# Kernel tuning notes

Measured on AMD Instinct MI355X. Metric: run time of the kernel, lower is better.

Reference implementation:

```python
import jax, jax.numpy as jnp
import numpy as np

D_MODEL = 1024
N_HEADS = 16


def setup_inputs() -> dict:
    key = jax.random.key(0)
    ks = jax.random.split(key, 5)
    B, T, C = 4, 2048, D_MODEL
    x = jax.random.normal(ks[0], (B, T, C), dtype=jnp.float32)
    W_attn = jax.random.normal(ks[1], (C, 3 * C), dtype=jnp.float32) * (1.0 / np.sqrt(C))
    b_attn = jnp.zeros((3 * C,), dtype=jnp.float32)
    W_proj = jax.random.normal(ks[2], (C, C), dtype=jnp.float32) * (1.0 / np.sqrt(C))
    b_proj = jnp.zeros((C,), dtype=jnp.float32)
    return {"x": x, "W_attn": W_attn, "b_attn": b_attn, "W_proj": W_proj, "b_proj": b_proj}


def reference(x, W_attn, b_attn, W_proj, b_proj):
    B, T, C = x.shape
    H = N_HEADS
    hd = C // H
    qkv = x @ W_attn + b_attn                      # [B,T,3C]
    q, k, v = jnp.split(qkv, 3, axis=2)
    # [B,T,C] -> [B,H,T,hd]
    q = q.reshape(B, T, H, hd).transpose(0, 2, 1, 3)
    k = k.reshape(B, T, H, hd).transpose(0, 2, 1, 3)
    v = v.reshape(B, T, H, hd).transpose(0, 2, 1, 3)
    scale = 1.0 / jnp.sqrt(jnp.float32(hd))
    attn = jnp.einsum('bhqd,bhkd->bhqk', q, k) * scale
    causal = jnp.tril(jnp.ones((T, T), dtype=bool))
    attn = jnp.where(causal[None, None], attn, -jnp.inf)
    w = jax.nn.softmax(attn, axis=-1)
    ctx = jnp.einsum('bhqk,bhkd->bhqd', w, v)      # [B,H,T,hd]
    ctx = ctx.transpose(0, 2, 1, 3).reshape(B, T, C)
    return ctx @ W_proj + b_proj
```

## Files before the change

### kernel.cpp

```cpp
#include <hip/hip_runtime.h>
#include <hip/hip_bf16.h>

typedef __bf16 bf16x8 __attribute__((ext_vector_type(8)));
typedef __bf16 bf16x4 __attribute__((ext_vector_type(4)));
typedef float f32x4 __attribute__((ext_vector_type(4)));

#define MFMA(A, B, C) __builtin_amdgcn_mfma_f32_16x16x32_bf16((A), (B), (C), 0, 0, 0)

#if __has_builtin(__builtin_amdgcn_exp2f)
#define EXP2(x) __builtin_amdgcn_exp2f(x)
#else
#define EXP2(x) exp2f(x)
#endif

#define T_SEQ 2048
#define BATCH 4
#define CDIM  1024
#define HEADS 16
#define HD    64
#define MROWS (BATCH * T_SEQ)
#define QK_SCALE 0.18033688011112042f
#define KTILES (CDIM / 64)

__device__ __forceinline__ void async_ld16(const __bf16* g, __bf16* l) {
    __builtin_amdgcn_global_load_lds(
        (const __attribute__((address_space(1))) void*)g,
        (__attribute__((address_space(3))) void*)l, 16, 0, 0);
}

__global__ __launch_bounds__(256) void prep(const float* __restrict__ x,
                                            __bf16* __restrict__ xbf,
                                            const float* __restrict__ Wa,
                                            __bf16* __restrict__ Wat,
                                            const float* __restrict__ Wp,
                                            __bf16* __restrict__ qkv)
{
    __shared__ float tile[32][33];
    const int bid = blockIdx.x;
    if (bid < 4096) {
        long i = ((long)bid * 256 + threadIdx.x) * 8;
        f32x4 f0 = ((const f32x4*)(x + i))[0];
        f32x4 f1 = ((const f32x4*)(x + i))[1];
        bf16x8 v;
#pragma unroll
        for (int j = 0; j < 4; j++) { v[j] = (__bf16)f0[j]; v[4 + j] = (__bf16)f1[j]; }
        *(bf16x8*)(xbf + i) = v;
    } else if (bid < 7168) {
        const int bb = bid - 4096;
        const int tx = threadIdx.x & 31, ty = threadIdx.x >> 5;
        const int c0 = (bb % 96) * 32, r0 = (bb / 96) * 32;
#pragma unroll
        for (int i = 0; i < 4; i++)
            tile[ty + i * 8][tx] = Wa[(long)(r0 + ty + i * 8) * (3 * CDIM) + c0 + tx];
        __syncthreads();
#pragma unroll
        for (int i = 0; i < 4; i++)
            Wat[(long)(c0 + ty + i * 8) * CDIM + r0 + tx] = (__bf16)tile[tx][ty + i * 8];
    } else {
        const int bb = bid - 7168;
        const int tx = threadIdx.x & 31, ty = threadIdx.x >> 5;
        const int c0 = (bb % 32) * 32, r0 = (bb / 32) * 32;
#pragma unroll
        for (int i = 0; i < 4; i++)
            tile[ty + i * 8][tx] = Wp[(long)(r0 + ty + i * 8) * CDIM + c0 + tx];
        __syncthreads();
#pragma unroll
        for (int i = 0; i < 4; i++)
            qkv[(long)(c0 + ty + i * 8) * (3 * CDIM) + 2 * CDIM + r0 + tx] =
                (__bf16)tile[tx][ty + i * 8];
    }
}


#define QS_ALO(p, kt)                                                            \
    do {                                                                         \
        async_ld16(Asrc + (long)(kt) * 64, &Ab[p][sdst]);                        \
        async_ld16(Asrc + (long)128 * CDIM + (kt) * 64, &Ab[p][8192 + sdst]);    \
    } while (0)
#define QS_AHI(p, kt)                                                            \
    do {                                                                         \
        async_ld16(Asrc + (long)64 * CDIM + (kt) * 64, &Ab[p][4096 + sdst]);     \
        async_ld16(Asrc + (long)192 * CDIM + (kt) * 64, &Ab[p][12288 + sdst]);   \
    } while (0)
#define QS_B(p, kt)                                                              \
    do {                                                                         \
        async_ld16(Bsrc + (long)(kt) * 64, &Bb[p][sdst]);                        \
        async_ld16(Bsrc + (long)64 * CDIM + (kt) * 64, &Bb[p][4096 + sdst]);     \
        async_ld16(Bsrc + (long)128 * CDIM + (kt) * 64, &Bb[p][8192 + sdst]);    \
    } while (0)

__global__ __launch_bounds__(512, 2) void gemm_qkv(const __bf16* __restrict__ A,
                                                   const __bf16* __restrict__ Bt,
                                                   const float* __restrict__ bias,
                                                   __bf16* __restrict__ C,
                                                   __bf16* __restrict__ vt)
{
    __shared__ __attribute__((aligned(16))) __bf16 Ab[2][256 * 64];
    __shared__ __attribute__((aligned(16))) __bf16 Bb[2][192 * 64];

    const int bid = (int)blockIdx.x;
    const int swz = (bid & 7) * 64 + (bid >> 3);
    const int n0 = (swz & 15) * 192;
    const int m0 = (swz >> 4) * 256;

    const int t = threadIdx.x;
    const int wave = t >> 6, lane = t & 63;
    const int quad = lane >> 4, l15 = lane & 15;
    const int wm = wave >> 2, wn = wave & 3;

    const int srow = t >> 3;
    const int scol = ((t & 7) * 8) ^ ((srow & 7) << 3);
    const int sdst = srow * 64 + (t & 7) * 8;
    const __bf16* Asrc = A + (long)(m0 + srow) * CDIM + scol;
    const __bf16* Bsrc = Bt + (long)(n0 + srow) * CDIM + scol;

    const int kx0 = (quad * 8) ^ ((l15 & 7) << 3);
    const int kx1 = (32 + quad * 8) ^ ((l15 & 7) << 3);
    const int aro = (wm * 128 + l15) * 64;
    const int bro = (wn * 48 + l15) * 64;

    f32x4 acc[8][3] = {};
    bf16x8 A0[4][2], A1[4][2], B0[2][2], B1[2];

    QS_ALO(0, 0); QS_AHI(0, 0); QS_B(0, 0);
    QS_ALO(1, 1); QS_AHI(1, 1); QS_B(1, 1);
    asm volatile("s_waitcnt vmcnt(7)" ::: "memory");
    __builtin_amdgcn_s_barrier();
#pragma unroll
    for (int mf = 0; mf < 4; mf++) {
        A0[mf][0] = *(const bf16x8*)&Ab[0][aro + mf * 1024 + kx0];
        A0[mf][1] = *(const bf16x8*)&Ab[0][aro + mf * 1024 + kx1];
    }
#pragma unroll
    for (int nf = 0; nf < 2; nf++) {
        B0[nf][0] = *(const bf16x8*)&Bb[0][bro + nf * 1024 + kx0];
        B0[nf][1] = *(const bf16x8*)&Bb[0][bro + nf * 1024 + kx1];
    }

#pragma unroll 2
    for (int kt = 0; kt < KTILES; ++kt) {
        const int cur = kt & 1, nxt = cur ^ 1;

#pragma unroll
        for (int mf = 0; mf < 4; mf++) {
            A1[mf][0] = *(const bf16x8*)&Ab[cur][aro + 4096 + mf * 1024 + kx0];
            A1[mf][1] = *(const bf16x8*)&Ab[cur][aro + 4096 + mf * 1024 + kx1];
        }
        __builtin_amdgcn_s_barrier();
        asm volatile("s_waitcnt lgkmcnt(8)");
        __builtin_amdgcn_sched_barrier(0);
        __builtin_amdgcn_s_setprio(1);
#pragma unroll
        for (int mf = 0; mf < 4; mf++)
#pragma unroll
            for (int nf = 0; nf < 2; nf++) {
                acc[mf][nf] = MFMA(A0[mf][0], B0[nf][0], acc[mf][nf]);
                acc[mf][nf] = MFMA(A0[mf][1], B0[nf][1], acc[mf][nf]);
            }
        __builtin_amdgcn_s_setprio(0);
        __builtin_amdgcn_s_barrier();

        B1[0] = *(const bf16x8*)&Bb[cur][bro + 2048 + kx0];
        B1[1] = *(const bf16x8*)&Bb[cur][bro + 2048 + kx1];
        if (kt + 2 < KTILES) QS_ALO(cur, kt + 2);
        __builtin_amdgcn_s_barrier();
        asm volatile("s_waitcnt lgkmcnt(2)");
        __builtin_amdgcn_sched_barrier(0);
        __builtin_amdgcn_s_setprio(1);
#pragma unroll
        for (int mf = 0; mf < 4; mf++)
#pragma unroll
            for (int nf = 0; nf < 2; nf++) {
                acc[4 + mf][nf] = MFMA(A1[mf][0], B0[nf][0], acc[4 + mf][nf]);
                acc[4 + mf][nf] = MFMA(A1[mf][1], B0[nf][1], acc[4 + mf][nf]);
            }
        __builtin_amdgcn_s_setprio(0);
        if (kt + 2 < KTILES) { asm volatile("s_waitcnt vmcnt(2)" ::: "memory"); }
        else                 { asm volatile("s_waitcnt vmcnt(0)" ::: "memory"); }
        __builtin_amdgcn_s_barrier();

        if (kt + 2 < KTILES) QS_AHI(cur, kt + 2);
        if (kt + 1 < KTILES) {
#pragma unroll
            for (int nf = 0; nf < 2; nf++) {
                B0[nf][0] = *(const bf16x8*)&Bb[nxt][bro + nf * 1024 + kx0];
                B0[nf][1] = *(const bf16x8*)&Bb[nxt][bro + nf * 1024 + kx1];
            }
        }
        __builtin_amdgcn_s_barrier();
        asm volatile("s_waitcnt lgkmcnt(4)");
        __builtin_amdgcn_sched_barrier(0);
        __builtin_amdgcn_s_setprio(1);
#pragma unroll
        for (int mf = 0; mf < 4; mf++) {
            acc[mf][2] = MFMA(A0[mf][0], B1[0], acc[mf][2]);
            acc[mf][2] = MFMA(A0[mf][1], B1[1], acc[mf][2]);
        }
        __builtin_amdgcn_s_setprio(0);
        __builtin_amdgcn_s_barrier();

        if (kt + 2 < KTILES) QS_B(cur, kt + 2);
        if (kt + 1 < KTILES) {
#pragma unroll
            for (int mf = 0; mf < 4; mf++) {
                A0[mf][0] = *(const bf16x8*)&Ab[nxt][aro + mf * 1024 + kx0];
                A0[mf][1] = *(const bf16x8*)&Ab[nxt][aro + mf * 1024 + kx1];
            }
        }
        __builtin_amdgcn_s_barrier();
        asm volatile("s_waitcnt lgkmcnt(8)");
        __builtin_amdgcn_sched_barrier(0);
        __builtin_amdgcn_s_setprio(1);
#pragma unroll
        for (int mf = 0; mf < 4; mf++) {
            acc[4 + mf][2] = MFMA(A1[mf][0], B1[0], acc[4 + mf][2]);
            acc[4 + mf][2] = MFMA(A1[mf][1], B1[1], acc[4 + mf][2]);
        }
        __builtin_amdgcn_s_setprio(0);
        __builtin_amdgcn_s_barrier();
    }

    const int bB = m0 >> 11;
    const int tb = (m0 & (T_SEQ - 1)) + wm * 128;
#pragma unroll
    for (int mf = 0; mf < 8; mf++) {
#pragma unroll
        for (int nf = 0; nf < 3; nf++) {
            const int colb = n0 + wn * 48 + nf * 16;
            const int col = colb + l15;
            const float bv = bias[col];
            if (colb >= 2 * CDIM) {
                __bf16* vdst = vt + (long)(bB * CDIM + col - 2 * CDIM) * T_SEQ
                             + tb + (mf >> 2) * 64 + (mf & 3) * 16 + quad * 4;
                bf16x4 pv;
#pragma unroll
                for (int r = 0; r < 4; r++) pv[r] = (__bf16)(acc[mf][nf][r] + bv);
                *(bf16x4*)vdst = pv;
            } else {
                const float sc = (col < CDIM) ? QK_SCALE : 1.0f;
#pragma unroll
                for (int r = 0; r < 4; r++) {
                    const int row = m0 + wm * 128 + (mf >> 2) * 64 + (mf & 3) * 16 + quad * 4 + r;
                    C[(long)row * (3 * CDIM) + col] = (__bf16)((acc[mf][nf][r] + bv) * sc);
                }
            }
        }
    }
}

#define PS_A(p, kt)                                                              \
    do {                                                                         \
        async_ld16(Asrc + (long)(kt) * 64, &Ab[p][sdst]);                        \
        async_ld16(Asrc + (long)64 * (3 * CDIM) + (kt) * 64, &Ab[p][4096 + sdst]); \
    } while (0)
#define PS_B(p, kt)                                                              \
    do {                                                                         \
        async_ld16(Bsrc + (long)(kt) * 64, &Bb[p][sdst]);                        \
        async_ld16(Bsrc + (long)64 * (3 * CDIM) + (kt) * 64, &Bb[p][4096 + sdst]); \
        async_ld16(Bsrc + (long)128 * (3 * CDIM) + (kt) * 64, &Bb[p][8192 + sdst]); \
        async_ld16(Bsrc + (long)192 * (3 * CDIM) + (kt) * 64, &Bb[p][12288 + sdst]); \
    } while (0)

__global__ __launch_bounds__(512, 2) void gemm_proj(const __bf16* __restrict__ A,
                                                    const float* __restrict__ bias,
                                                    float* __restrict__ C)
{
    __shared__ __attribute__((aligned(16))) __bf16 Ab[2][128 * 64];
    __shared__ __attribute__((aligned(16))) __bf16 Bb[2][256 * 64];

    const int bid = (int)blockIdx.x;
    const int swz = (bid & 7) * 32 + (bid >> 3);
    const int n0 = (swz & 3) * 256;
    const int m0 = (swz >> 2) * 128;

    const int t = threadIdx.x;
    const int wave = t >> 6, lane = t & 63;
    const int quad = lane >> 4, l15 = lane & 15;
    const int wm = wave >> 2, wn = wave & 3;

    const int srow = t >> 3;
    const int scol = ((t & 7) * 8) ^ ((srow & 7) << 3);
    const int sdst = srow * 64 + (t & 7) * 8;
    const __bf16* Asrc = A + (long)(m0 + srow) * (3 * CDIM) + scol;
    const __bf16* Bsrc = A + (long)(n0 + srow) * (3 * CDIM) + 2 * CDIM + scol;

    const int kx0 = (quad * 8) ^ ((l15 & 7) << 3);
    const int kx1 = (32 + quad * 8) ^ ((l15 & 7) << 3);
    const int aro = (wm * 64 + l15) * 64;
    const int bro = (wn * 64 + l15) * 64;

    f32x4 acc[4][4] = {};
    bf16x8 A0[2][2], A1[2][2], B0[2][2], B1[2][2];

    PS_A(0, 0); PS_B(0, 0);
    PS_A(1, 1); PS_B(1, 1);
    asm volatile("s_waitcnt vmcnt(6)" ::: "memory");
    __builtin_amdgcn_s_barrier();
#pragma unroll
    for (int mf = 0; mf < 2; mf++) {
        A0[mf][0] = *(const bf16x8*)&Ab[0][aro + mf * 1024 + kx0];
        A0[mf][1] = *(const bf16x8*)&Ab[0][aro + mf * 1024 + kx1];
    }
#pragma unroll
    for (int nf = 0; nf < 2; nf++) {
        B0[nf][0] = *(const bf16x8*)&Bb[0][bro + nf * 1024 + kx0];
        B0[nf][1] = *(const bf16x8*)&Bb[0][bro + nf * 1024 + kx1];
    }

#pragma unroll 2
    for (int kt = 0; kt < KTILES; ++kt) {
        const int cur = kt & 1, nxt = cur ^ 1;

#pragma unroll
        for (int mf = 0; mf < 2; mf++) {
            A1[mf][0] = *(const bf16x8*)&Ab[cur][aro + 2048 + mf * 1024 + kx0];
            A1[mf][1] = *(const bf16x8*)&Ab[cur][aro + 2048 + mf * 1024 + kx1];
        }
        __builtin_amdgcn_s_barrier();
        asm volatile("s_waitcnt lgkmcnt(4)");
        __builtin_amdgcn_sched_barrier(0);
        __builtin_amdgcn_s_setprio(1);
#pragma unroll
        for (int mf = 0; mf < 2; mf++)
#pragma unroll
            for (int nf = 0; nf < 2; nf++) {
                acc[mf][nf] = MFMA(A0[mf][0], B0[nf][0], acc[mf][nf]);
                acc[mf][nf] = MFMA(A0[mf][1], B0[nf][1], acc[mf][nf]);
            }
        __builtin_amdgcn_s_setprio(0);
        __builtin_amdgcn_s_barrier();

#pragma unroll
        for (int nf = 0; nf < 2; nf++) {
            B1[nf][0] = *(const bf16x8*)&Bb[cur][bro + 2048 + nf * 1024 + kx0];
            B1[nf][1] = *(const bf16x8*)&Bb[cur][bro + 2048 + nf * 1024 + kx1];
        }
        __builtin_amdgcn_s_barrier();
        asm volatile("s_waitcnt lgkmcnt(4)");
        __builtin_amdgcn_sched_barrier(0);
        __builtin_amdgcn_s_setprio(1);
#pragma unroll
        for (int mf = 0; mf < 2; mf++)
#pragma unroll
            for (int nf = 0; nf < 2; nf++) {
                acc[2 + mf][nf] = MFMA(A1[mf][0], B0[nf][0], acc[2 + mf][nf]);
                acc[2 + mf][nf] = MFMA(A1[mf][1], B0[nf][1], acc[2 + mf][nf]);
            }
        __builtin_amdgcn_s_setprio(0);
        asm volatile("s_waitcnt vmcnt(0)" ::: "memory");
        __builtin_amdgcn_s_barrier();

        if (kt + 2 < KTILES) PS_A(cur, kt + 2);
        if (kt + 1 < KTILES) {
#pragma unroll
            for (int nf = 0; nf < 2; nf++) {
                B0[nf][0] = *(const bf16x8*)&Bb[nxt][bro + nf * 1024 + kx0];
                B0[nf][1] = *(const bf16x8*)&Bb[nxt][bro + nf * 1024 + kx1];
            }
        }
        __builtin_amdgcn_s_barrier();
        asm volatile("s_waitcnt lgkmcnt(4)");
        __builtin_amdgcn_sched_barrier(0);
        __builtin_amdgcn_s_setprio(1);
#pragma unroll
        for (int mf = 0; mf < 2; mf++)
#pragma unroll
            for (int nf = 0; nf < 2; nf++) {
                acc[mf][2 + nf] = MFMA(A0[mf][0], B1[nf][0], acc[mf][2 + nf]);
                acc[mf][2 + nf] = MFMA(A0[mf][1], B1[nf][1], acc[mf][2 + nf]);
            }
        __builtin_amdgcn_s_setprio(0);
        __builtin_amdgcn_s_barrier();

        if (kt + 2 < KTILES) PS_B(cur, kt + 2);
        if (kt + 1 < KTILES) {
#pragma unroll
            for (int mf = 0; mf < 2; mf++) {
                A0[mf][0] = *(const bf16x8*)&Ab[nxt][aro + mf * 1024 + kx0];
                A0[mf][1] = *(const bf16x8*)&Ab[nxt][aro + mf * 1024 + kx1];
            }
        }
        __builtin_amdgcn_s_barrier();
        asm volatile("s_waitcnt lgkmcnt(4)");
        __builtin_amdgcn_sched_barrier(0);
        __builtin_amdgcn_s_setprio(1);
#pragma unroll
        for (int mf = 0; mf < 2; mf++)
#pragma unroll
            for (int nf = 0; nf < 2; nf++) {
                acc[2 + mf][2 + nf] = MFMA(A1[mf][0], B1[nf][0], acc[2 + mf][2 + nf]);
                acc[2 + mf][2 + nf] = MFMA(A1[mf][1], B1[nf][1], acc[2 + mf][2 + nf]);
            }
        __builtin_amdgcn_s_setprio(0);
        __builtin_amdgcn_s_barrier();
    }

#pragma unroll
    for (int mf = 0; mf < 4; mf++) {
#pragma unroll
        for (int nf = 0; nf < 4; nf++) {
            const int col = n0 + wn * 64 + (nf >> 1) * 32 + (nf & 1) * 16 + l15;
            const float bv = bias[col];
#pragma unroll
            for (int r = 0; r < 4; r++) {
                const int row = m0 + wm * 64 + (mf >> 1) * 32 + (mf & 1) * 16 + quad * 4 + r;
                C[(long)row * CDIM + col] = acc[mf][nf][r] + bv;
            }
        }
    }
}

__global__ __launch_bounds__(256) void attn_kernel(__bf16* qkv,
                                                   const __bf16* __restrict__ vt)
{
    __shared__ __attribute__((aligned(16))) __bf16 Ks[2][64 * 32];
    __shared__ __attribute__((aligned(16))) __bf16 Vts[2][64 * 32];
    __shared__ __attribute__((aligned(16))) __bf16 Ps[8][16 * 72];

    const int bh = blockIdx.x;
    const int b = bh >> 4, h = bh & 15;
    const int qt = (int)gridDim.y - 1 - (int)blockIdx.y;
    const int q0 = qt * 128;
    const int t = threadIdx.x;
    const int wave = t >> 6, lane = t & 63;
    const int quad = lane >> 4, l15 = lane & 15;

    bf16x8 qfr[2][2];
#pragma unroll
    for (int f = 0; f < 2; f++) {
        const __bf16* qb = qkv + (long)(b * T_SEQ + q0 + f * 64 + wave * 16 + l15) * (3 * CDIM) + h * HD;
        qfr[f][0] = *(const bf16x8*)(qb + quad * 8);
        qfr[f][1] = *(const bf16x8*)(qb + 32 + quad * 8);
    }

    bf16x8 vone;
#pragma unroll
    for (int j = 0; j < 8; j++) vone[j] = (__bf16)1.0f;

    f32x4 Oacc[2][4] = {};
    f32x4 lacc[2] = {};

    const __bf16* kbase = qkv + (long)(b * T_SEQ + (t >> 2)) * (3 * CDIM)
                          + CDIM + h * HD + (t & 3) * 8;
    const __bf16* vbase = vt + ((long)bh * HD + (t >> 2)) * T_SEQ + (t & 3) * 8;

    const int ntiles = (q0 + 128) / 64;
    for (int kt = 0; kt < ntiles; kt++) {
        const __bf16* kp = kbase + (long)kt * 64 * (3 * CDIM);
        async_ld16(kp,      &Ks[0][t * 8]);
        async_ld16(kp + 32, &Ks[1][t * 8]);
        const __bf16* vp = vbase + kt * 64;
        async_ld16(vp,      &Vts[0][t * 8]);
        async_ld16(vp + 32, &Vts[1][t * 8]);
        __syncthreads();

#pragma unroll
        for (int c = 0; c < 4; c++) {
            bf16x8 kf0 = *(const bf16x8*)&Ks[0][(c * 16 + l15) * 32 + quad * 8];
            bf16x8 kf1 = *(const bf16x8*)&Ks[1][(c * 16 + l15) * 32 + quad * 8];
#pragma unroll
            for (int f = 0; f < 2; f++) {
                f32x4 z = {};
                z = MFMA(kf0, qfr[f][0], z);
                z = MFMA(kf1, qfr[f][1], z);
                const int qbf = q0 + f * 64 + wave * 16;
                const int qg = qbf + l15;
                const int kvb = kt * 64 + c * 16 + quad * 4;
                bf16x4 pk;
                if (kt * 64 + 63 > qbf) {
#pragma unroll
                    for (int r = 0; r < 4; r++) {
                        float v = (kvb + r > qg) ? -1e30f : z[r];
                        pk[r] = (__bf16)EXP2(v);
                    }
                } else {
#pragma unroll
                    for (int r = 0; r < 4; r++)
                        pk[r] = (__bf16)EXP2(z[r]);
                }
                *(bf16x4*)&Ps[wave * 2 + f][l15 * 72 + c * 16 + quad * 4] = pk;
            }
        }

        __threadfence_block();

        bf16x8 pf[2][2];
#pragma unroll
        for (int f = 0; f < 2; f++) {
            pf[f][0] = *(const bf16x8*)&Ps[wave * 2 + f][l15 * 72 + quad * 8];
            pf[f][1] = *(const bf16x8*)&Ps[wave * 2 + f][l15 * 72 + 32 + quad * 8];
            lacc[f] = MFMA(pf[f][0], vone, lacc[f]);
            lacc[f] = MFMA(pf[f][1], vone, lacc[f]);
        }
#pragma unroll
        for (int n = 0; n < 4; n++) {
            bf16x8 vf0 = *(const bf16x8*)&Vts[0][(n * 16 + l15) * 32 + quad * 8];
            bf16x8 vf1 = *(const bf16x8*)&Vts[1][(n * 16 + l15) * 32 + quad * 8];
#pragma unroll
            for (int f = 0; f < 2; f++) {
                Oacc[f][n] = MFMA(pf[f][0], vf0, Oacc[f][n]);
                Oacc[f][n] = MFMA(pf[f][1], vf1, Oacc[f][n]);
            }
        }
        __syncthreads();
    }

#pragma unroll
    for (int f = 0; f < 2; f++)
#pragma unroll
        for (int n = 0; n < 4; n++) {
            int col = h * HD + n * 16 + l15;
#pragma unroll
            for (int r = 0; r < 4; r++) {
                int row = q0 + f * 64 + wave * 16 + quad * 4 + r;
                float val = Oacc[f][n][r] / lacc[f][r];
                qkv[(long)(b * T_SEQ + row) * (3 * CDIM) + col] = (__bf16)val;
            }
        }
}

extern "C" void kernel_launch(void* const* d_in, const int* in_sizes, int n_in,
                              void* d_out, int out_size, void* d_ws, size_t ws_size,
                              hipStream_t stream) {
    (void)in_sizes; (void)n_in; (void)out_size; (void)ws_size;
    const float* x  = (const float*)d_in[0];
    const float* Wa = (const float*)d_in[1];
    const float* ba = (const float*)d_in[2];
    const float* Wp = (const float*)d_in[3];
    const float* bp = (const float*)d_in[4];
    float* out = (float*)d_out;

    char* ws = (char*)d_ws;
    __bf16* qkv = (__bf16*)(ws);
    __bf16* vt  = (__bf16*)(ws + 50331648);
    __bf16* xbf = (__bf16*)d_out;
    __bf16* Wat = (__bf16*)((char*)d_out + 16777216);

    prep<<<dim3(8192), 256, 0, stream>>>(x, xbf, Wa, Wat, Wp, qkv);

    gemm_qkv<<<dim3(512), 512, 0, stream>>>(xbf, Wat, ba, qkv, vt);

    attn_kernel<<<dim3(BATCH * HEADS, T_SEQ / 128), 256, 0, stream>>>(qkv, vt);

    gemm_proj<<<dim3(256), 512, 0, stream>>>(qkv, bp, out);
}
```

Measured before the change: 251.1 us.

## Collapse GEMM main-loop phases to a single barrier per k-tile

In both the QKV and output-projection GEMM main loops, the per-tile multi-phase schedule (many s_barriers interleaved with partial LDS reads and global-to-LDS prefetches) is replaced by one workgroup barrier per k-tile. All LDS fragment reads for the current tile are issued before the MFMA groups. The next tile's fragments and all global-to-LDS prefetches for tile kt+2 are then issued together after the barrier. This is meant to cut barrier stalls between waves. In exchange, the QKV kernel now waits vmcnt(0) instead of vmcnt(2), and the finer interleaving of memory traffic with MFMA work is lost.

```diff
diff --git a/kernel.cpp b/kernel.cpp
--- a/kernel.cpp
+++ b/kernel.cpp
@@ -146,8 +146,9 @@
             A1[mf][0] = *(const bf16x8*)&Ab[cur][aro + 4096 + mf * 1024 + kx0];
             A1[mf][1] = *(const bf16x8*)&Ab[cur][aro + 4096 + mf * 1024 + kx1];
         }
-        __builtin_amdgcn_s_barrier();
-        asm volatile("s_waitcnt lgkmcnt(8)");
+        B1[0] = *(const bf16x8*)&Bb[cur][bro + 2048 + kx0];
+        B1[1] = *(const bf16x8*)&Bb[cur][bro + 2048 + kx1];
+        asm volatile("s_waitcnt lgkmcnt(10)" ::: "memory");
         __builtin_amdgcn_sched_barrier(0);
         __builtin_amdgcn_s_setprio(1);
 #pragma unroll
@@ -158,13 +159,7 @@
                 acc[mf][nf] = MFMA(A0[mf][1], B0[nf][1], acc[mf][nf]);
             }
         __builtin_amdgcn_s_setprio(0);
-        __builtin_amdgcn_s_barrier();
-
-        B1[0] = *(const bf16x8*)&Bb[cur][bro + 2048 + kx0];
-        B1[1] = *(const bf16x8*)&Bb[cur][bro + 2048 + kx1];
-        if (kt + 2 < KTILES) QS_ALO(cur, kt + 2);
-        __builtin_amdgcn_s_barrier();
-        asm volatile("s_waitcnt lgkmcnt(2)");
+        asm volatile("s_waitcnt lgkmcnt(0)" ::: "memory");
         __builtin_amdgcn_sched_barrier(0);
         __builtin_amdgcn_s_setprio(1);
 #pragma unroll
@@ -175,21 +170,9 @@
                 acc[4 + mf][nf] = MFMA(A1[mf][1], B0[nf][1], acc[4 + mf][nf]);
             }
         __builtin_amdgcn_s_setprio(0);
-        if (kt + 2 < KTILES) { asm volatile("s_waitcnt vmcnt(2)" ::: "memory"); }
-        else                 { asm volatile("s_waitcnt vmcnt(0)" ::: "memory"); }
+        asm volatile("s_waitcnt vmcnt(0)" ::: "memory");
         __builtin_amdgcn_s_barrier();
 
-        if (kt + 2 < KTILES) QS_AHI(cur, kt + 2);
-        if (kt + 1 < KTILES) {
-#pragma unroll
-            for (int nf = 0; nf < 2; nf++) {
-                B0[nf][0] = *(const bf16x8*)&Bb[nxt][bro + nf * 1024 + kx0];
-                B0[nf][1] = *(const bf16x8*)&Bb[nxt][bro + nf * 1024 + kx1];
-            }
-        }
-        __builtin_amdgcn_s_barrier();
-        asm volatile("s_waitcnt lgkmcnt(4)");
-        __builtin_amdgcn_sched_barrier(0);
         __builtin_amdgcn_s_setprio(1);
 #pragma unroll
         for (int mf = 0; mf < 4; mf++) {
@@ -197,19 +180,19 @@
             acc[mf][2] = MFMA(A0[mf][1], B1[1], acc[mf][2]);
         }
         __builtin_amdgcn_s_setprio(0);
-        __builtin_amdgcn_s_barrier();
-
-        if (kt + 2 < KTILES) QS_B(cur, kt + 2);
         if (kt + 1 < KTILES) {
 #pragma unroll
             for (int mf = 0; mf < 4; mf++) {
                 A0[mf][0] = *(const bf16x8*)&Ab[nxt][aro + mf * 1024 + kx0];
                 A0[mf][1] = *(const bf16x8*)&Ab[nxt][aro + mf * 1024 + kx1];
             }
-        }
-        __builtin_amdgcn_s_barrier();
-        asm volatile("s_waitcnt lgkmcnt(8)");
-        __builtin_amdgcn_sched_barrier(0);
+#pragma unroll
+            for (int nf = 0; nf < 2; nf++) {
+                B0[nf][0] = *(const bf16x8*)&Bb[nxt][bro + nf * 1024 + kx0];
+                B0[nf][1] = *(const bf16x8*)&Bb[nxt][bro + nf * 1024 + kx1];
+            }
+        }
+        if (kt + 2 < KTILES) { QS_ALO(cur, kt + 2); QS_AHI(cur, kt + 2); QS_B(cur, kt + 2); }
         __builtin_amdgcn_s_setprio(1);
 #pragma unroll
         for (int mf = 0; mf < 4; mf++) {
@@ -217,7 +200,6 @@
             acc[4 + mf][2] = MFMA(A1[mf][1], B1[1], acc[4 + mf][2]);
         }
         __builtin_amdgcn_s_setprio(0);
-        __builtin_amdgcn_s_barrier();
     }
 
     const int bB = m0 >> 11;
@@ -316,27 +298,23 @@
             A1[mf][0] = *(const bf16x8*)&Ab[cur][aro + 2048 + mf * 1024 + kx0];
             A1[mf][1] = *(const bf16x8*)&Ab[cur][aro + 2048 + mf * 1024 + kx1];
         }
-        __builtin_amdgcn_s_barrier();
-        asm volatile("s_waitcnt lgkmcnt(4)");
-        __builtin_amdgcn_sched_barrier(0);
-        __builtin_amdgcn_s_setprio(1);
-#pragma unroll
-        for (int mf = 0; mf < 2; mf++)
-#pragma unroll
-            for (int nf = 0; nf < 2; nf++) {
-                acc[mf][nf] = MFMA(A0[mf][0], B0[nf][0], acc[mf][nf]);
-                acc[mf][nf] = MFMA(A0[mf][1], B0[nf][1], acc[mf][nf]);
-            }
-        __builtin_amdgcn_s_setprio(0);
-        __builtin_amdgcn_s_barrier();
-
 #pragma unroll
         for (int nf = 0; nf < 2; nf++) {
             B1[nf][0] = *(const bf16x8*)&Bb[cur][bro + 2048 + nf * 1024 + kx0];
             B1[nf][1] = *(const bf16x8*)&Bb[cur][bro + 2048 + nf * 1024 + kx1];
         }
-        __builtin_amdgcn_s_barrier();
-        asm volatile("s_waitcnt lgkmcnt(4)");
+        asm volatile("s_waitcnt lgkmcnt(8)" ::: "memory");
+        __builtin_amdgcn_sched_barrier(0);
+        __builtin_amdgcn_s_setprio(1);
+#pragma unroll
+        for (int mf = 0; mf < 2; mf++)
+#pragma unroll
+            for (int nf = 0; nf < 2; nf++) {
+                acc[mf][nf] = MFMA(A0[mf][0], B0[nf][0], acc[mf][nf]);
+                acc[mf][nf] = MFMA(A0[mf][1], B0[nf][1], acc[mf][nf]);
+            }
+        __builtin_amdgcn_s_setprio(0);
+        asm volatile("s_waitcnt lgkmcnt(0)" ::: "memory");
         __builtin_amdgcn_sched_barrier(0);
         __builtin_amdgcn_s_setprio(1);
 #pragma unroll
@@ -350,17 +328,6 @@
         asm volatile("s_waitcnt vmcnt(0)" ::: "memory");
         __builtin_amdgcn_s_barrier();
 
-        if (kt + 2 < KTILES) PS_A(cur, kt + 2);
-        if (kt + 1 < KTILES) {
-#pragma unroll
-            for (int nf = 0; nf < 2; nf++) {
-                B0[nf][0] = *(const bf16x8*)&Bb[nxt][bro + nf * 1024 + kx0];
-                B0[nf][1] = *(const bf16x8*)&Bb[nxt][bro + nf * 1024 + kx1];
-            }
-        }
-        __builtin_amdgcn_s_barrier();
-        asm volatile("s_waitcnt lgkmcnt(4)");
-        __builtin_amdgcn_sched_barrier(0);
         __builtin_amdgcn_s_setprio(1);
 #pragma unroll
         for (int mf = 0; mf < 2; mf++)
@@ -370,19 +337,19 @@
                 acc[mf][2 + nf] = MFMA(A0[mf][1], B1[nf][1], acc[mf][2 + nf]);
             }
         __builtin_amdgcn_s_setprio(0);
-        __builtin_amdgcn_s_barrier();
-
-        if (kt + 2 < KTILES) PS_B(cur, kt + 2);
         if (kt + 1 < KTILES) {
 #pragma unroll
             for (int mf = 0; mf < 2; mf++) {
                 A0[mf][0] = *(const bf16x8*)&Ab[nxt][aro + mf * 1024 + kx0];
                 A0[mf][1] = *(const bf16x8*)&Ab[nxt][aro + mf * 1024 + kx1];
             }
-        }
-        __builtin_amdgcn_s_barrier();
-        asm volatile("s_waitcnt lgkmcnt(4)");
-        __builtin_amdgcn_sched_barrier(0);
+#pragma unroll
+            for (int nf = 0; nf < 2; nf++) {
+                B0[nf][0] = *(const bf16x8*)&Bb[nxt][bro + nf * 1024 + kx0];
+                B0[nf][1] = *(const bf16x8*)&Bb[nxt][bro + nf * 1024 + kx1];
+            }
+        }
+        if (kt + 2 < KTILES) { PS_A(cur, kt + 2); PS_B(cur, kt + 2); }
         __builtin_amdgcn_s_setprio(1);
 #pragma unroll
         for (int mf = 0; mf < 2; mf++)
@@ -392,7 +359,6 @@
                 acc[2 + mf][2 + nf] = MFMA(A1[mf][1], B1[nf][1], acc[2 + mf][2 + nf]);
             }
         __builtin_amdgcn_s_setprio(0);
-        __builtin_amdgcn_s_barrier();
     }
 
 #pragma unroll
```

Result: faster. 230.6 us (-8.2%).
